# Performance work log

Hardware: AMD Instinct MI355X
Metric: run time of the kernel (lower is better)

Reference implementation:

```python
import jax, jax.numpy as jnp
import numpy as np

B, S, D = 4, 2048, 1024
H = 8  # hardcoded in AttentionLayer
HD = D // H
FF = 4096
EPS = 1e-5


def _layernorm(x):
    # LayerNorm(hidden_dim, elementwise_affine=False), eps=1e-5
    mu = jnp.mean(x, axis=-1, keepdims=True)
    var = jnp.var(x, axis=-1, keepdims=True)
    return (x - mu) / jnp.sqrt(var + EPS)


def setup_inputs() -> dict:
    key = jax.random.key(0)
    ks = jax.random.split(key, 5)
    scale = 0.02
    return {
        "x": jax.random.normal(ks[0], (B, S, D), dtype=jnp.float32),
        "qkv_proj": jax.random.normal(ks[1], (D, 3 * D), dtype=jnp.float32) * scale,
        "o_proj": jax.random.normal(ks[2], (D, D), dtype=jnp.float32) * scale,
        "ff1": jax.random.normal(ks[3], (D, FF), dtype=jnp.float32) * scale,
        "ff2": jax.random.normal(ks[4], (FF, D), dtype=jnp.float32) * scale,
    }


def reference(x, qkv_proj, o_proj, ff1, ff2):
    b, s, d = x.shape
    # --- attention ---
    qkv = jnp.matmul(x, qkv_proj)                       # [b,s,3d]
    qkv = qkv.reshape(b, s, H, 3 * HD).transpose(0, 2, 1, 3)  # [b,h,s,3hd]
    q, k, v = jnp.split(qkv, 3, axis=-1)                # each [b,h,s,hd]
    logits = jnp.einsum('bhqd,bhkd->bhqk', q, k) / jnp.sqrt(jnp.float32(HD))
    attn = jax.nn.softmax(logits, axis=-1)
    vals = jnp.einsum('bhqk,bhkd->bhqd', attn, v)       # [b,h,s,hd]
    vals = vals.transpose(0, 2, 1, 3).reshape(b, s, d)
    attn_out = jnp.matmul(vals, o_proj)
    # --- residual + norm + FFN + residual + norm ---
    x = _layernorm(x + attn_out)
    ff_out = jnp.matmul(jax.nn.relu(jnp.matmul(x, ff1)), ff2)
    x = _layernorm(x + ff_out)
    return x
```

## Files before the change

### kernel.cpp

```cpp
#include <hip/hip_runtime.h>
#include <hip/hip_bf16.h>


typedef float floatx4 __attribute__((ext_vector_type(4)));
typedef float floatx16 __attribute__((ext_vector_type(16)));
typedef short bf16x8 __attribute__((ext_vector_type(8)));

#define DEVI __device__ __forceinline__

typedef const __attribute__((address_space(1))) unsigned int* gas1_t;
typedef __attribute__((address_space(3))) unsigned int* las3_t;

DEVI void gll16(const void* g, void* l) {
  __builtin_amdgcn_global_load_lds((gas1_t)g, (las3_t)l, 16, 0, 0);
}

DEVI short bfbits(float f) {
  __hip_bfloat16 h = __float2bfloat16(f);
  return *reinterpret_cast<short*>(&h);
}

template<int EPI, int SPLITK>
__global__ __launch_bounds__(256, 4) void gemm_bt(
    const __hip_bfloat16* __restrict__ A,
    const __hip_bfloat16* __restrict__ BT,
    float* __restrict__ Cf, float* __restrict__ Cf2,
    __hip_bfloat16* __restrict__ Cb,
    int M, int N, int K)
{
  __shared__ __hip_bfloat16 As[128 * 64];
  __shared__ __hip_bfloat16 Bs[128 * 64];
  const int tid = threadIdx.x;
  const int wave = tid >> 6, lane = tid & 63;
  const int lane15 = lane & 15, quad = lane >> 4;
  const int row0 = blockIdx.x * 128, col0 = blockIdx.y * 128;
  const int wr = (wave >> 1) * 64, wc = (wave & 1) * 64;
  const int Kh = K / SPLITK;
  const size_t kofs = (SPLITK > 1) ? (size_t)blockIdx.z * Kh : 0;

  floatx4 acc[4][4] = {};

  const int srow = tid >> 3;
  const int sblk = (tid & 7) ^ (srow & 7);
  const __hip_bfloat16* Ag = A + (size_t)(row0 + srow) * K + kofs + sblk * 8;
  const __hip_bfloat16* Bg = BT + (size_t)(col0 + srow) * K + kofs + sblk * 8;
  char* Asl = (char*)As + tid * 16;
  char* Bsl = (char*)Bs + tid * 16;
  const size_t rstep = (size_t)32 * K;

  const int x7 = lane15 & 7;
  for (int k0 = 0; k0 < Kh; k0 += 64) {
    __syncthreads();
#pragma unroll
    for (int p = 0; p < 4; p++) {
      gll16(Ag + k0 + p * rstep, Asl + p * 4096);
      gll16(Bg + k0 + p * rstep, Bsl + p * 4096);
    }
    __syncthreads();
#pragma unroll
    for (int kc = 0; kc < 2; kc++) {
      bf16x8 af[4], bb[4];
#pragma unroll
      for (int t = 0; t < 4; t++) {
        const int r = wr + t * 16 + lane15;
        af[t] = *(const bf16x8*)((const char*)As + r * 128 + (((kc * 4 + quad) ^ x7) << 4));
      }
#pragma unroll
      for (int t = 0; t < 4; t++) {
        const int r = wc + t * 16 + lane15;
        bb[t] = *(const bf16x8*)((const char*)Bs + r * 128 + (((kc * 4 + quad) ^ x7) << 4));
      }
#pragma unroll
      for (int i = 0; i < 4; i++)
#pragma unroll
        for (int j = 0; j < 4; j++)
          acc[i][j] = __builtin_amdgcn_mfma_f32_16x16x32_bf16(af[i], bb[j], acc[i][j], 0, 0, 0);
    }
  }

  float* Cp = (SPLITK > 1 && blockIdx.z) ? Cf2 : Cf;
#pragma unroll
  for (int i = 0; i < 4; i++) {
    const int mb = row0 + wr + i * 16 + quad * 4;
#pragma unroll
    for (int j = 0; j < 4; j++) {
      const int n = col0 + wc + j * 16 + lane15;
#pragma unroll
      for (int r = 0; r < 4; r++) {
        const size_t idx = (size_t)(mb + r) * N + n;
        const float v = acc[i][j][r];
        if (EPI == 0) {
          Cb[idx] = __float2bfloat16(v);
        } else if (EPI == 2) {
          Cb[idx] = __float2bfloat16(v > 0.f ? v : 0.f);
        } else {
          Cp[idx] = v;
        }
      }
    }
  }
}

__global__ __launch_bounds__(256, 2) void attn_kernel(
    const __hip_bfloat16* __restrict__ qkv,
    const __hip_bfloat16* __restrict__ Vt,
    __hip_bfloat16* __restrict__ vals)
{
  __shared__ __hip_bfloat16 KVs[128 * 128];
  __shared__ __hip_bfloat16 QP[128 * 128];

  const int tid = threadIdx.x;
  const int wave = tid >> 6, lane = tid & 63;
  const int l31 = lane & 31, l5 = lane >> 5;
  const int qt = blockIdx.x, bh = blockIdx.y;
  const int b = bh >> 3, h = bh & 7;
  const size_t tokbase = (size_t)b * 2048;
  const float scale = 0.08838834764831845f;

  const int sw8 = ((tid & 15) ^ (tid >> 4)) * 8;
  const int srow = tid >> 4;
  const __hip_bfloat16* qg  = qkv + (tokbase + qt * 128) * 3072 + h * 384 + sw8;
  const __hip_bfloat16* kg0 = qkv + tokbase * 3072 + h * 384 + 128 + sw8;
  const __hip_bfloat16* vg0 = Vt + (size_t)bh * 128 * 2048 + sw8;

#pragma unroll
  for (int rd = 0; rd < 8; rd++)
    gll16(qg + (size_t)(rd * 16 + srow) * 3072, (char*)QP + rd * 4096 + tid * 16);
  __syncthreads();

  const int rx = l31 & 15;
  bf16x8 qf[8];
  {
    const char* qb = (const char*)QP + (wave * 32 + l31) * 256;
#pragma unroll
    for (int ks = 0; ks < 8; ks++)
      qf[ks] = *(const bf16x8*)(qb + (((ks * 2 + l5) ^ rx) << 4));
  }

  floatx16 oacc[4] = {};
  float lsum[16];
#pragma unroll
  for (int r = 0; r < 16; r++) lsum[r] = 0.f;

  for (int kt = 0; kt < 16; kt++) {
    __syncthreads();
#pragma unroll
    for (int rd = 0; rd < 8; rd++)
      gll16(kg0 + (size_t)(kt * 128 + rd * 16 + srow) * 3072,
            (char*)KVs + rd * 4096 + tid * 16);
    __syncthreads();

    floatx16 sacc[4] = {};
#pragma unroll
    for (int ks = 0; ks < 8; ks++) {
      const char* kb = (const char*)KVs + l31 * 256 + (((ks * 2 + l5) ^ rx) << 4);
#pragma unroll
      for (int nt = 0; nt < 4; nt++) {
        const bf16x8 bk = *(const bf16x8*)(kb + nt * 8192);
        sacc[nt] = __builtin_amdgcn_mfma_f32_32x32x16_bf16(qf[ks], bk, sacc[nt], 0, 0, 0);
      }
    }

    const int pbase = wave * 8192 + l5 * 1024 + (l31 & 7) * 2;
#pragma unroll
    for (int g = 0; g < 4; g++) {
      const int hgx = l5 + 2 * (g & 1);
#pragma unroll
      for (int r3 = 0; r3 < 4; r3++) {
        const int r = g * 4 + r3;
        const int rowoff = (r3 << 8) + (g << 11) + ((((l31 >> 3) ^ r3)) << 4);
        float part = 0.f;
#pragma unroll
        for (int t = 0; t < 4; t++) {
          const float p = __expf(sacc[t][r] * scale);
          part += p;
          *(short*)((char*)QP + pbase + rowoff + ((t ^ hgx) << 6)) = bfbits(p);
        }
        lsum[r] += part;
      }
    }

    __syncthreads();
#pragma unroll
    for (int rd = 0; rd < 8; rd++)
      gll16(vg0 + (size_t)kt * 128 + (size_t)(rd * 16 + srow) * 2048,
            (char*)KVs + rd * 4096 + tid * 16);
    __syncthreads();

#pragma unroll
    for (int ks = 0; ks < 8; ks++) {
      const bf16x8 ap = *(const bf16x8*)((const char*)QP +
          (wave * 32 + l31) * 256 + (((ks * 2 + l5) ^ rx) << 4));
      const char* vb = (const char*)KVs + l31 * 256 + (((ks * 2 + l5) ^ rx) << 4);
#pragma unroll
      for (int nt = 0; nt < 4; nt++) {
        const bf16x8 bv = *(const bf16x8*)(vb + nt * 8192);
        oacc[nt] = __builtin_amdgcn_mfma_f32_32x32x16_bf16(ap, bv, oacc[nt], 0, 0, 0);
      }
    }
  }

#pragma unroll
  for (int r = 0; r < 16; r++) {
#pragma unroll
    for (int off = 1; off < 32; off <<= 1)
      lsum[r] += __shfl_xor(lsum[r], off);
  }

  const size_t orow0 = tokbase + (size_t)qt * 128 + wave * 32;
#pragma unroll
  for (int g = 0; g < 4; g++) {
#pragma unroll
    for (int r3 = 0; r3 < 4; r3++) {
      const int r = g * 4 + r3;
      const float linv = 1.f / lsum[r];
      const size_t row = orow0 + r3 + 8 * g + 4 * l5;
#pragma unroll
      for (int nt = 0; nt < 4; nt++)
        vals[row * 1024 + h * 128 + nt * 32 + l31] =
            __float2bfloat16(oacc[nt][r] * linv);
    }
  }
}

__global__ __launch_bounds__(256) void cvt_bf16_k(const float* __restrict__ in,
                                                  __hip_bfloat16* __restrict__ out) {
  const size_t i = (size_t)blockIdx.x * 256 + threadIdx.x;
  const float4 v = ((const float4*)in)[i];
  short4 sv;
  sv.x = bfbits(v.x); sv.y = bfbits(v.y); sv.z = bfbits(v.z); sv.w = bfbits(v.w);
  ((short4*)out)[i] = sv;
}

__global__ __launch_bounds__(256) void wtrans_k(const float* __restrict__ W,
                                                __hip_bfloat16* __restrict__ WT,
                                                int K, int N) {
  __shared__ float t[32][33];
  const int tx = threadIdx.x & 31, ty = threadIdx.x >> 5;
  const int n0 = blockIdx.x * 32, k0 = blockIdx.y * 32;
#pragma unroll
  for (int i = 0; i < 4; i++)
    t[ty + i * 8][tx] = W[(size_t)(k0 + ty + i * 8) * N + n0 + tx];
  __syncthreads();
#pragma unroll
  for (int i = 0; i < 4; i++)
    WT[(size_t)(n0 + ty + i * 8) * K + k0 + tx] = __float2bfloat16(t[tx][ty + i * 8]);
}

__global__ __launch_bounds__(256) void vtrans_k(const __hip_bfloat16* __restrict__ qkv,
                                                __hip_bfloat16* __restrict__ Vt) {
  __shared__ __hip_bfloat16 t[32][33];
  const int tx = threadIdx.x & 31, ty = threadIdx.x >> 5;
  const int s0 = blockIdx.x * 32, d0 = blockIdx.y * 32, bh = blockIdx.z;
  const int b = bh >> 3, h = bh & 7;
#pragma unroll
  for (int i = 0; i < 4; i++)
    t[ty + i * 8][tx] = qkv[((size_t)b * 2048 + s0 + ty + i * 8) * 3072 + h * 384 + 256 + d0 + tx];
  __syncthreads();
#pragma unroll
  for (int i = 0; i < 4; i++)
    Vt[((size_t)bh * 128 + d0 + ty + i * 8) * 2048 + s0 + tx] = t[tx][ty + i * 8];
}

template<bool RES_BF16, bool FINAL>
__global__ __launch_bounds__(256) void ln_red_k(
    const float* __restrict__ p0, const float* __restrict__ p1,
    const float* __restrict__ resf, const __hip_bfloat16* __restrict__ resb,
    __hip_bfloat16* __restrict__ ob, float* __restrict__ of) {
  const int row = blockIdx.x, tid = threadIdx.x;
  const size_t base = (size_t)row * 1024;
  const float4 a = ((const float4*)(p0 + base))[tid];
  const float4 bb = ((const float4*)(p1 + base))[tid];
  float4 v;
  if (RES_BF16) {
    const short4 rb = ((const short4*)(resb + base))[tid];
    v.x = a.x + bb.x + __bfloat162float(*(const __hip_bfloat16*)&rb.x);
    v.y = a.y + bb.y + __bfloat162float(*(const __hip_bfloat16*)&rb.y);
    v.z = a.z + bb.z + __bfloat162float(*(const __hip_bfloat16*)&rb.z);
    v.w = a.w + bb.w + __bfloat162float(*(const __hip_bfloat16*)&rb.w);
  } else {
    const float4 rf = ((const float4*)(resf + base))[tid];
    v.x = a.x + bb.x + rf.x; v.y = a.y + bb.y + rf.y;
    v.z = a.z + bb.z + rf.z; v.w = a.w + bb.w + rf.w;
  }
  float s = v.x + v.y + v.z + v.w;
  float q = v.x * v.x + v.y * v.y + v.z * v.z + v.w * v.w;
#pragma unroll
  for (int off = 32; off; off >>= 1) { s += __shfl_xor(s, off); q += __shfl_xor(q, off); }
  __shared__ float ss[4], sq[4];
  const int wave = tid >> 6;
  if ((tid & 63) == 0) { ss[wave] = s; sq[wave] = q; }
  __syncthreads();
  s = ss[0] + ss[1] + ss[2] + ss[3];
  q = sq[0] + sq[1] + sq[2] + sq[3];
  const float mean = s * (1.f / 1024.f);
  const float var = q * (1.f / 1024.f) - mean * mean;
  const float rstd = rsqrtf(var + 1e-5f);
  float4 o;
  o.x = (v.x - mean) * rstd; o.y = (v.y - mean) * rstd;
  o.z = (v.z - mean) * rstd; o.w = (v.w - mean) * rstd;
  if (FINAL) {
    ((float4*)(of + base))[tid] = o;
  } else {
    short4 sv;
    sv.x = bfbits(o.x); sv.y = bfbits(o.y); sv.z = bfbits(o.z); sv.w = bfbits(o.w);
    ((short4*)(ob + base))[tid] = sv;
  }
}

extern "C" void kernel_launch(void* const* d_in, const int* in_sizes, int n_in,
                              void* d_out, int out_size, void* d_ws, size_t ws_size,
                              hipStream_t stream) {
  const float* x    = (const float*)d_in[0];
  const float* qkvw = (const float*)d_in[1];
  const float* ow   = (const float*)d_in[2];
  const float* f1   = (const float*)d_in[3];
  const float* f2   = (const float*)d_in[4];
  float* out = (float*)d_out;

  char* ws = (char*)d_ws;
  const size_t MB = 1024 * 1024;
  __hip_bfloat16* xb   = (__hip_bfloat16*)(ws);
  __hip_bfloat16* vals = xb;
  float*          P1f  = (float*)(ws);
  __hip_bfloat16* qkvT = (__hip_bfloat16*)(ws + 16 * MB);
  __hip_bfloat16* oT   = (__hip_bfloat16*)(ws + 22 * MB);
  __hip_bfloat16* f1T  = (__hip_bfloat16*)(ws + 24 * MB);
  __hip_bfloat16* f2T  = (__hip_bfloat16*)(ws + 32 * MB);
  __hip_bfloat16* qkvb = (__hip_bfloat16*)(ws + 40 * MB);
  __hip_bfloat16* Vt   = (__hip_bfloat16*)(ws + 88 * MB);
  float*          P0o  = (float*)(ws + 40 * MB);
  float*          P1o  = (float*)(ws + 72 * MB);
  __hip_bfloat16* hmid = (__hip_bfloat16*)(ws + 40 * MB);
  float*          P0f  = (float*)(ws + 104 * MB);
  __hip_bfloat16* x1b  = (__hip_bfloat16*)(ws + 136 * MB);
  (void)in_sizes; (void)n_in; (void)out_size; (void)ws_size;

  cvt_bf16_k<<<8192, 256, 0, stream>>>(x, xb);
  wtrans_k<<<dim3(96, 32), 256, 0, stream>>>(qkvw, qkvT, 1024, 3072);
  wtrans_k<<<dim3(32, 32), 256, 0, stream>>>(ow, oT, 1024, 1024);
  wtrans_k<<<dim3(128, 32), 256, 0, stream>>>(f1, f1T, 1024, 4096);
  wtrans_k<<<dim3(32, 128), 256, 0, stream>>>(f2, f2T, 4096, 1024);
  gemm_bt<0, 1><<<dim3(64, 24, 1), 256, 0, stream>>>(xb, qkvT, nullptr, nullptr,
                                                     qkvb, 8192, 3072, 1024);
  vtrans_k<<<dim3(64, 4, 32), 256, 0, stream>>>(qkvb, Vt);
  attn_kernel<<<dim3(16, 32), 256, 0, stream>>>(qkvb, Vt, vals);
  gemm_bt<4, 2><<<dim3(64, 8, 2), 256, 0, stream>>>(vals, oT, P0o, P1o,
                                                    nullptr, 8192, 1024, 1024);
  ln_red_k<false, false><<<8192, 256, 0, stream>>>(P0o, P1o, x, nullptr, x1b, nullptr);
  gemm_bt<2, 1><<<dim3(64, 32, 1), 256, 0, stream>>>(x1b, f1T, nullptr, nullptr,
                                                     hmid, 8192, 4096, 1024);
  gemm_bt<4, 2><<<dim3(64, 8, 2), 256, 0, stream>>>(hmid, f2T, P0f, P1f,
                                                    nullptr, 8192, 1024, 4096);
  ln_red_k<true, true><<<8192, 256, 0, stream>>>(P0f, P1f, nullptr, x1b, nullptr, out);
}
```

Before: 490.0 us.

## Transpose attention MFMAs to keep P in registers and double-buffer K/V loads

Swaps MFMA operand order so scores come out as S^T, which lets the softmax probabilities be packed to bf16 and exchanged between half-waves with shuffles instead of being written to shared memory. This frees the Q buffer to hold V, so the V tile load is issued before the QK^T compute and the next K tile is prefetched during the PV compute, which removes two barriers per iteration and overlaps loads with math. Row sums collapse to a single per-lane scalar, and outputs are stored as short4 vectors. It adds shuffle traffic and register pressure, and correctness depends on the lane/fragment mapping being exactly right.

```diff
diff --git a/kernel.cpp b/kernel.cpp
--- a/kernel.cpp
+++ b/kernel.cpp
@@ -106,8 +106,8 @@
     const __hip_bfloat16* __restrict__ Vt,
     __hip_bfloat16* __restrict__ vals)
 {
-  __shared__ __hip_bfloat16 KVs[128 * 128];
-  __shared__ __hip_bfloat16 QP[128 * 128];
+  __shared__ __hip_bfloat16 Ak[128 * 128];
+  __shared__ __hip_bfloat16 Bq[128 * 128];
 
   const int tid = threadIdx.x;
   const int wave = tid >> 6, lane = tid & 63;
@@ -125,102 +125,112 @@
 
 #pragma unroll
   for (int rd = 0; rd < 8; rd++)
-    gll16(qg + (size_t)(rd * 16 + srow) * 3072, (char*)QP + rd * 4096 + tid * 16);
+    gll16(qg + (size_t)(rd * 16 + srow) * 3072, (char*)Bq + rd * 4096 + tid * 16);
   __syncthreads();
 
   const int rx = l31 & 15;
   bf16x8 qf[8];
   {
-    const char* qb = (const char*)QP + (wave * 32 + l31) * 256;
+    const char* qb = (const char*)Bq + (wave * 32 + l31) * 256;
 #pragma unroll
     for (int ks = 0; ks < 8; ks++)
       qf[ks] = *(const bf16x8*)(qb + (((ks * 2 + l5) ^ rx) << 4));
   }
+#pragma unroll
+  for (int rd = 0; rd < 8; rd++)
+    gll16(kg0 + (size_t)(rd * 16 + srow) * 3072, (char*)Ak + rd * 4096 + tid * 16);
+  __syncthreads();
 
   floatx16 oacc[4] = {};
-  float lsum[16];
-#pragma unroll
-  for (int r = 0; r < 16; r++) lsum[r] = 0.f;
+  float lsum = 0.f;
 
   for (int kt = 0; kt < 16; kt++) {
-    __syncthreads();
-#pragma unroll
-    for (int rd = 0; rd < 8; rd++)
-      gll16(kg0 + (size_t)(kt * 128 + rd * 16 + srow) * 3072,
-            (char*)KVs + rd * 4096 + tid * 16);
-    __syncthreads();
-
-    floatx16 sacc[4] = {};
-#pragma unroll
-    for (int ks = 0; ks < 8; ks++) {
-      const char* kb = (const char*)KVs + l31 * 256 + (((ks * 2 + l5) ^ rx) << 4);
-#pragma unroll
-      for (int nt = 0; nt < 4; nt++) {
-        const bf16x8 bk = *(const bf16x8*)(kb + nt * 8192);
-        sacc[nt] = __builtin_amdgcn_mfma_f32_32x32x16_bf16(qf[ks], bk, sacc[nt], 0, 0, 0);
-      }
-    }
-
-    const int pbase = wave * 8192 + l5 * 1024 + (l31 & 7) * 2;
-#pragma unroll
-    for (int g = 0; g < 4; g++) {
-      const int hgx = l5 + 2 * (g & 1);
-#pragma unroll
-      for (int r3 = 0; r3 < 4; r3++) {
-        const int r = g * 4 + r3;
-        const int rowoff = (r3 << 8) + (g << 11) + ((((l31 >> 3) ^ r3)) << 4);
-        float part = 0.f;
-#pragma unroll
-        for (int t = 0; t < 4; t++) {
-          const float p = __expf(sacc[t][r] * scale);
-          part += p;
-          *(short*)((char*)QP + pbase + rowoff + ((t ^ hgx) << 6)) = bfbits(p);
-        }
-        lsum[r] += part;
-      }
-    }
-
-    __syncthreads();
+    if (kt) __syncthreads();
+
 #pragma unroll
     for (int rd = 0; rd < 8; rd++)
       gll16(vg0 + (size_t)kt * 128 + (size_t)(rd * 16 + srow) * 2048,
-            (char*)KVs + rd * 4096 + tid * 16);
+            (char*)Bq + rd * 4096 + tid * 16);
+
+    floatx16 sacc[4] = {};
+#pragma unroll
+    for (int ks = 0; ks < 8; ks++) {
+      const int off = ((ks * 2 + l5) ^ rx) << 4;
+      const char* kb = (const char*)Ak + l31 * 256 + off;
+#pragma unroll
+      for (int nt = 0; nt < 4; nt++) {
+        const bf16x8 ak = *(const bf16x8*)(kb + nt * 8192);
+        sacc[nt] = __builtin_amdgcn_mfma_f32_32x32x16_bf16(ak, qf[ks], sacc[nt], 0, 0, 0);
+      }
+    }
+
+    unsigned int pk0[16], pk1[16];
+#pragma unroll
+    for (int idx = 0; idx < 16; idx++) {
+      const int nt = idx >> 2, g4 = (idx & 3) * 4;
+      const float p0 = __expf(sacc[nt][g4 + 0] * scale);
+      const float p1 = __expf(sacc[nt][g4 + 1] * scale);
+      const float p2 = __expf(sacc[nt][g4 + 2] * scale);
+      const float p3 = __expf(sacc[nt][g4 + 3] * scale);
+      lsum += (p0 + p1) + (p2 + p3);
+      pk0[idx] = (unsigned int)(unsigned short)bfbits(p0) |
+                 ((unsigned int)(unsigned short)bfbits(p1) << 16);
+      pk1[idx] = (unsigned int)(unsigned short)bfbits(p2) |
+                 ((unsigned int)(unsigned short)bfbits(p3) << 16);
+    }
+    bf16x8 pf[8];
+#pragma unroll
+    for (int ks = 0; ks < 8; ks++) {
+      const unsigned int own0 = l5 ? pk0[ks * 2 + 1] : pk0[ks * 2];
+      const unsigned int own1 = l5 ? pk1[ks * 2 + 1] : pk1[ks * 2];
+      const unsigned int snd0 = l5 ? pk0[ks * 2] : pk0[ks * 2 + 1];
+      const unsigned int snd1 = l5 ? pk1[ks * 2] : pk1[ks * 2 + 1];
+      const unsigned int rc0 = (unsigned int)__shfl_xor((int)snd0, 32);
+      const unsigned int rc1 = (unsigned int)__shfl_xor((int)snd1, 32);
+      union { int4 i; bf16x8 v; } u;
+      u.i.x = l5 ? (int)rc0 : (int)own0;
+      u.i.y = l5 ? (int)rc1 : (int)own1;
+      u.i.z = l5 ? (int)own0 : (int)rc0;
+      u.i.w = l5 ? (int)own1 : (int)rc1;
+      pf[ks] = u.v;
+    }
+
     __syncthreads();
+    if (kt < 15) {
+#pragma unroll
+      for (int rd = 0; rd < 8; rd++)
+        gll16(kg0 + (size_t)((kt + 1) * 128 + rd * 16 + srow) * 3072,
+              (char*)Ak + rd * 4096 + tid * 16);
+    }
 
 #pragma unroll
     for (int ks = 0; ks < 8; ks++) {
-      const bf16x8 ap = *(const bf16x8*)((const char*)QP +
-          (wave * 32 + l31) * 256 + (((ks * 2 + l5) ^ rx) << 4));
-      const char* vb = (const char*)KVs + l31 * 256 + (((ks * 2 + l5) ^ rx) << 4);
+      const int off = ((ks * 2 + l5) ^ rx) << 4;
+      const char* vb = (const char*)Bq + l31 * 256 + off;
 #pragma unroll
       for (int nt = 0; nt < 4; nt++) {
-        const bf16x8 bv = *(const bf16x8*)(vb + nt * 8192);
-        oacc[nt] = __builtin_amdgcn_mfma_f32_32x32x16_bf16(ap, bv, oacc[nt], 0, 0, 0);
-      }
-    }
-  }
-
-#pragma unroll
-  for (int r = 0; r < 16; r++) {
-#pragma unroll
-    for (int off = 1; off < 32; off <<= 1)
-      lsum[r] += __shfl_xor(lsum[r], off);
-  }
-
-  const size_t orow0 = tokbase + (size_t)qt * 128 + wave * 32;
-#pragma unroll
-  for (int g = 0; g < 4; g++) {
-#pragma unroll
-    for (int r3 = 0; r3 < 4; r3++) {
-      const int r = g * 4 + r3;
-      const float linv = 1.f / lsum[r];
-      const size_t row = orow0 + r3 + 8 * g + 4 * l5;
-#pragma unroll
-      for (int nt = 0; nt < 4; nt++)
-        vals[row * 1024 + h * 128 + nt * 32 + l31] =
-            __float2bfloat16(oacc[nt][r] * linv);
-    }
-  }
+        const bf16x8 av = *(const bf16x8*)(vb + nt * 8192);
+        oacc[nt] = __builtin_amdgcn_mfma_f32_32x32x16_bf16(av, pf[ks], oacc[nt], 0, 0, 0);
+      }
+    }
+  }
+
+  lsum += __shfl_xor(lsum, 32);
+  const float linv = 1.f / lsum;
+
+  const size_t row = tokbase + (size_t)qt * 128 + wave * 32 + l31;
+  __hip_bfloat16* vrow = vals + row * 1024 + h * 128 + 4 * l5;
+#pragma unroll
+  for (int nt = 0; nt < 4; nt++)
+#pragma unroll
+    for (int g = 0; g < 4; g++) {
+      short4 sv;
+      sv.x = bfbits(oacc[nt][g * 4 + 0] * linv);
+      sv.y = bfbits(oacc[nt][g * 4 + 1] * linv);
+      sv.z = bfbits(oacc[nt][g * 4 + 2] * linv);
+      sv.w = bfbits(oacc[nt][g * 4 + 3] * linv);
+      *(short4*)(vrow + nt * 32 + g * 8) = sv;
+    }
 }
 
 __global__ __launch_bounds__(256) void cvt_bf16_k(const float* __restrict__ in,
```

Measured after the change: 500.6 us. +2.2%, slower.
